# Kernel optimization log

Measured on AMD Instinct MI355X. Metric: run time of the kernel, lower is better.

Reference implementation:

```python
import jax, jax.numpy as jnp
import numpy as np


COMMITMENT_COST = 0.25


def setup_inputs() -> dict:
    key = jax.random.key(0)
    k1, k2 = jax.random.split(key)
    B, C, H, W = 16, 128, 64, 64
    K = 1024
    z = jax.random.normal(k1, (B, C, H, W), dtype=jnp.float32)
    # original init: uniform(-1/K, 1/K); keep that scale for faithfulness
    codebook = jax.random.uniform(k2, (K, C), dtype=jnp.float32,
                                  minval=-1.0 / K, maxval=1.0 / K)
    return {"z": z, "codebook": codebook}


def reference(z, codebook):
    B, C, H, W = z.shape
    K = codebook.shape[0]
    # (B,C,H,W) -> (N,C) with N = B*H*W
    z_flat = jnp.transpose(z, (0, 2, 3, 1)).reshape(-1, C)
    # squared-distance matrix (N,K): ||z||^2 + ||e||^2 - 2 z.e
    dists = (jnp.sum(z_flat ** 2, axis=1, keepdims=True)
             + jnp.sum(codebook ** 2, axis=1)
             - 2.0 * z_flat @ codebook.T)
    indices = jnp.argmin(dists, axis=1)  # (N,)
    z_q = jnp.transpose(codebook[indices].reshape(B, H, W, C), (0, 3, 1, 2))
    commitment_loss = jnp.mean((jax.lax.stop_gradient(z_q) - z) ** 2)
    codebook_loss = jnp.mean((z_q - jax.lax.stop_gradient(z)) ** 2)
    vq_loss = codebook_loss + COMMITMENT_COST * commitment_loss
    # straight-through estimator
    z_q_st = z + jax.lax.stop_gradient(z_q - z)
    usage = jnp.sum(jnp.bincount(indices, length=K) > 0).astype(jnp.float32) / K
    return (z_q_st, vq_loss, usage)
```

## Files before the change

kernel.cpp:

```cpp
#include <hip/hip_runtime.h>

typedef __attribute__((ext_vector_type(8))) short short8;
typedef __attribute__((ext_vector_type(4))) float f32x4;

#define C_DIM 128
#define K_CODES 1024
#define TOT 8388608
#define NBLK 512

__device__ __forceinline__ unsigned int f2bf1(float f) {
  unsigned int u = __float_as_uint(f);
  return (u + 0x7FFFu + ((u >> 16) & 1u)) >> 16;
}
__device__ __forceinline__ unsigned int f2bf2(float lo, float hi) {
  return f2bf1(lo) | (f2bf1(hi) << 16);
}

union U16x8 { uint4 u; short8 s; };

__global__ void prep_kernel(const float* __restrict__ cb,
                            unsigned short* __restrict__ ebf,
                            float* __restrict__ nsq1,
                            int* __restrict__ used) {
  int gid = blockIdx.x * 256 + threadIdx.x;
  const float4 v = ((const float4*)cb)[gid];
  uint2 pk;
  pk.x = f2bf2(v.x, v.y);
  pk.y = f2bf2(v.z, v.w);
  ((uint2*)ebf)[gid] = pk;
  if (gid < K_CODES) {
    float s = 0.f;
    #pragma unroll 8
    for (int c = 0; c < C_DIM; ++c) { float w = cb[gid * C_DIM + c]; s += w * w; }
    nsq1[gid] = 1.0f + s;
    used[gid] = 0;
  }
}

__global__ __launch_bounds__(512, 4)
void vq_main(const float* __restrict__ zin,
             const unsigned short* __restrict__ ebf,
             const float* __restrict__ nsq1,
             int* __restrict__ used, float* __restrict__ lossp,
             float* __restrict__ out) {
  __shared__ __align__(16) uint4 bG[2][1024];
  __shared__ float nsq_s[K_CODES];
  __shared__ unsigned int mergeK[128][2];
  __shared__ int   widx[128];
  __shared__ float wsum[8];

  const int t  = threadIdx.x;
  const int L  = t & 63;
  const int wv = t >> 6;
  const int ph = wv >> 1;
  const int kh = wv & 1;
  const int q  = L >> 4;
  const int nL = L & 15;

  const int bb = blockIdx.x >> 5;
  const int hg = blockIdx.x & 31;
  const int zoff = bb * (C_DIM * 4096) + hg * 128;

  for (int i = t; i < K_CODES; i += 512) nsq_s[i] = nsq1[i];

  short8 afrag[8];
  #pragma unroll
  for (int mt = 0; mt < 2; ++mt) {
    const int wcol = ph * 32 + mt * 16 + nL;
    #pragma unroll
    for (int ks = 0; ks < 4; ++ks) {
      float v[8];
      #pragma unroll
      for (int u = 0; u < 8; ++u)
        v[u] = zin[zoff + (ks * 32 + q * 8 + u) * 4096 + wcol];
      U16x8 pk;
      pk.u.x = f2bf2(-2.f * v[0], -2.f * v[1]);
      pk.u.y = f2bf2(-2.f * v[2], -2.f * v[3]);
      pk.u.z = f2bf2(-2.f * v[4], -2.f * v[5]);
      pk.u.w = f2bf2(-2.f * v[6], -2.f * v[7]);
      afrag[mt * 4 + ks] = pk.s;
    }
  }

  const uint4* __restrict__ ebv = (const uint4*)ebf;
  const int nLw = (t >> 4) & 15;
  const int oct = t & 15;
  const int pb  = t >> 8;
  const int sks = oct >> 2, sq = oct & 3;

  #pragma unroll
  for (int i = 0; i < 2; ++i) {
    int p = pb + 2 * i;
    bG[0][p * 256 + sks * 64 + nLw * 4 + sq] = ebv[(p * 16 + nLw) * 16 + oct];
  }
  __syncthreads();

  unsigned int kmin[8];
  #pragma unroll
  for (int i = 0; i < 8; ++i) kmin[i] = 0xFFFFFFFFu;

  #pragma unroll 1
  for (int ch = 0; ch < 16; ++ch) {
    const int cur = ch & 1;
    if (ch < 15) {
      #pragma unroll
      for (int i = 0; i < 2; ++i) {
        int p = pb + 2 * i;
        bG[cur ^ 1][p * 256 + sks * 64 + nLw * 4 + sq] =
            ebv[((ch + 1) * 64 + p * 16 + nLw) * 16 + oct];
      }
    }
    const short8* bp = (const short8*)bG[cur];
    #pragma unroll
    for (int j2 = 0; j2 < 2; ++j2) {
      const int jj = kh * 2 + j2;
      const int row = ch * 64 + jj * 16 + nL;
      short8 b0 = bp[jj * 256 + 0 * 64 + nL * 4 + q];
      short8 b1 = bp[jj * 256 + 1 * 64 + nL * 4 + q];
      short8 b2 = bp[jj * 256 + 2 * 64 + nL * 4 + q];
      short8 b3 = bp[jj * 256 + 3 * 64 + nL * 4 + q];
      const float nv = nsq_s[row];
      f32x4 c0 = {nv, nv, nv, nv};
      f32x4 c1 = {nv, nv, nv, nv};
      c0 = __builtin_amdgcn_mfma_f32_16x16x32_bf16(afrag[0], b0, c0, 0, 0, 0);
      c1 = __builtin_amdgcn_mfma_f32_16x16x32_bf16(afrag[4], b0, c1, 0, 0, 0);
      c0 = __builtin_amdgcn_mfma_f32_16x16x32_bf16(afrag[1], b1, c0, 0, 0, 0);
      c1 = __builtin_amdgcn_mfma_f32_16x16x32_bf16(afrag[5], b1, c1, 0, 0, 0);
      c0 = __builtin_amdgcn_mfma_f32_16x16x32_bf16(afrag[2], b2, c0, 0, 0, 0);
      c1 = __builtin_amdgcn_mfma_f32_16x16x32_bf16(afrag[6], b2, c1, 0, 0, 0);
      c0 = __builtin_amdgcn_mfma_f32_16x16x32_bf16(afrag[3], b3, c0, 0, 0, 0);
      c1 = __builtin_amdgcn_mfma_f32_16x16x32_bf16(afrag[7], b3, c1, 0, 0, 0);
      const unsigned int rowc = (unsigned int)row;
      #pragma unroll
      for (int r = 0; r < 4; ++r) {
        unsigned int k0 = (__float_as_uint(c0[r]) & 0xFFFFFC00u) | rowc;
        if (k0 < kmin[r]) kmin[r] = k0;
        unsigned int k1 = (__float_as_uint(c1[r]) & 0xFFFFFC00u) | rowc;
        if (k1 < kmin[4 + r]) kmin[4 + r] = k1;
      }
    }
    __syncthreads();
  }

  #pragma unroll
  for (int m = 1; m <= 8; m <<= 1) {
    #pragma unroll
    for (int i = 0; i < 8; ++i) {
      unsigned int o = (unsigned int)__shfl_xor((int)kmin[i], m, 64);
      if (o < kmin[i]) kmin[i] = o;
    }
  }
  if (nL == 0) {
    #pragma unroll
    for (int mt = 0; mt < 2; ++mt)
      #pragma unroll
      for (int r = 0; r < 4; ++r)
        mergeK[ph * 32 + mt * 16 + q * 4 + r][kh] = kmin[mt * 4 + r];
  }
  __syncthreads();

  if (t < 128) {
    unsigned int b = min(mergeK[t][0], mergeK[t][1]);
    int bi = (int)(b & 1023u);
    widx[t] = bi;
    used[bi] = 1;
  }
  __syncthreads();

  float lsum = 0.f;
  {
    const int p = t & 127, cg = t >> 7;
    const int idx = widx[p];
    const uint4* erow = ebv + idx * 16 + cg * 4;
    const int obase = zoff + cg * 32 * 4096 + p;
    #pragma unroll
    for (int i = 0; i < 4; ++i) {
      uint4 g = erow[i];
      const unsigned int wrd[4] = {g.x, g.y, g.z, g.w};
      #pragma unroll
      for (int half = 0; half < 4; ++half) {
        float e0 = __uint_as_float(wrd[half] << 16);
        float e1 = __uint_as_float(wrd[half] & 0xFFFF0000u);
        int off = obase + (i * 8 + half * 2) * 4096;
        float d0 = zin[off] - e0;
        out[off] = e0;
        lsum += d0 * d0;
        off += 4096;
        float d1 = zin[off] - e1;
        out[off] = e1;
        lsum += d1 * d1;
      }
    }
  }
  #pragma unroll
  for (int o = 32; o > 0; o >>= 1) lsum += __shfl_down(lsum, o, 64);
  if (L == 0) wsum[wv] = lsum;
  __syncthreads();
  if (t == 0)
    lossp[blockIdx.x] = ((wsum[0] + wsum[1]) + (wsum[2] + wsum[3]))
                      + ((wsum[4] + wsum[5]) + (wsum[6] + wsum[7]));
}

__global__ void finalize_kernel(const int* __restrict__ used,
                                const float* __restrict__ lossp,
                                float* __restrict__ out2) {
  __shared__ int   redi[256];
  __shared__ float redf[256];
  int t = threadIdx.x;
  int s = 0;
  for (int i = t; i < K_CODES; i += 256) s += (used[i] != 0) ? 1 : 0;
  float ls = 0.f;
  for (int i = t; i < NBLK; i += 256) ls += lossp[i];
  redi[t] = s; redf[t] = ls;
  __syncthreads();
  for (int o = 128; o > 0; o >>= 1) {
    if (t < o) { redi[t] += redi[t + o]; redf[t] += redf[t + o]; }
    __syncthreads();
  }
  if (t == 0) {
    out2[0] = 1.25f * redf[0] / (float)TOT;
    out2[1] = (float)redi[0] / 1024.0f;
  }
}

extern "C" void kernel_launch(void* const* d_in, const int* in_sizes, int n_in,
                              void* d_out, int out_size, void* d_ws, size_t ws_size,
                              hipStream_t stream) {
  const float* z  = (const float*)d_in[0];
  const float* cb = (const float*)d_in[1];
  float* out = (float*)d_out;
  char* ws = (char*)d_ws;
  unsigned short* ebf = (unsigned short*)ws;
  float* nsq1  = (float*)(ws + 262144);
  int*   used  = (int*)(ws + 266240);
  float* lossp = (float*)(ws + 270336);

  hipLaunchKernelGGL(prep_kernel, dim3(128), dim3(256), 0, stream,
                     cb, ebf, nsq1, used);
  hipLaunchKernelGGL(vq_main, dim3(NBLK), dim3(512), 0, stream,
                     z, ebf, nsq1, used, lossp, out);
  hipLaunchKernelGGL(finalize_kernel, dim3(1), dim3(256), 0, stream,
                     used, lossp, out + TOT);
}
```

Measured before the change: 116.9 us.

## Widen per-wave M tile to 64 rows and swizzle LDS codebook layout

Each wave now holds A fragments for 64 pixel columns (four M tiles) and covers one 16-code slice per chunk, instead of 32 columns and two code slices. Every B fragment read from LDS now feeds four MFMAs rather than two, which halves LDS read traffic per MFMA. The shared codebook tile is also stored with an XOR swizzle to cut bank conflicts, and the final argmin merge combines four partial results instead of two. In exchange, register pressure roughly doubles for A fragments, accumulators and kmin values, which could cause spills or reduce occupancy under the 512x4 launch bounds.

New measurement: 117.8 us. About the same (+0.8%).

```diff
diff --git a/kernel.cpp b/kernel.cpp
--- a/kernel.cpp
+++ b/kernel.cpp
@@ -45,15 +45,15 @@
              float* __restrict__ out) {
   __shared__ __align__(16) uint4 bG[2][1024];
   __shared__ float nsq_s[K_CODES];
-  __shared__ unsigned int mergeK[128][2];
+  __shared__ unsigned int mergeK[128][4];
   __shared__ int   widx[128];
   __shared__ float wsum[8];
 
   const int t  = threadIdx.x;
   const int L  = t & 63;
   const int wv = t >> 6;
-  const int ph = wv >> 1;
-  const int kh = wv & 1;
+  const int ph = wv >> 2;
+  const int kq = wv & 3;
   const int q  = L >> 4;
   const int nL = L & 15;
 
@@ -63,10 +63,10 @@
 
   for (int i = t; i < K_CODES; i += 512) nsq_s[i] = nsq1[i];
 
-  short8 afrag[8];
-  #pragma unroll
-  for (int mt = 0; mt < 2; ++mt) {
-    const int wcol = ph * 32 + mt * 16 + nL;
+  short8 afrag[16];
+  #pragma unroll
+  for (int mt = 0; mt < 4; ++mt) {
+    const int wcol = ph * 64 + mt * 16 + nL;
     #pragma unroll
     for (int ks = 0; ks < 4; ++ks) {
       float v[8];
@@ -87,17 +87,23 @@
   const int oct = t & 15;
   const int pb  = t >> 8;
   const int sks = oct >> 2, sq = oct & 3;
+  const int swbase = (nLw >> 1) * 8 + (((nLw ^ sks) & 1) << 2)
+                   + ((sq ^ (nLw >> 1)) & 3);
 
   #pragma unroll
   for (int i = 0; i < 2; ++i) {
     int p = pb + 2 * i;
-    bG[0][p * 256 + sks * 64 + nLw * 4 + sq] = ebv[(p * 16 + nLw) * 16 + oct];
-  }
-  __syncthreads();
-
-  unsigned int kmin[8];
-  #pragma unroll
-  for (int i = 0; i < 8; ++i) kmin[i] = 0xFFFFFFFFu;
+    bG[0][p * 256 + sks * 64 + swbase] = ebv[(p * 16 + nLw) * 16 + oct];
+  }
+  __syncthreads();
+
+  const int rdq = (q ^ (nL >> 1)) & 3;
+  const int sA = kq * 256 + (nL >> 1) * 8 + (((nL) & 1) << 2) + rdq;
+  const int sB = kq * 256 + (nL >> 1) * 8 + (((nL ^ 1) & 1) << 2) + rdq;
+
+  unsigned int kmin[16];
+  #pragma unroll
+  for (int i = 0; i < 16; ++i) kmin[i] = 0xFFFFFFFFu;
 
   #pragma unroll 1
   for (int ch = 0; ch < 16; ++ch) {
@@ -106,30 +112,38 @@
       #pragma unroll
       for (int i = 0; i < 2; ++i) {
         int p = pb + 2 * i;
-        bG[cur ^ 1][p * 256 + sks * 64 + nLw * 4 + sq] =
+        bG[cur ^ 1][p * 256 + sks * 64 + swbase] =
             ebv[((ch + 1) * 64 + p * 16 + nLw) * 16 + oct];
       }
     }
     const short8* bp = (const short8*)bG[cur];
-    #pragma unroll
-    for (int j2 = 0; j2 < 2; ++j2) {
-      const int jj = kh * 2 + j2;
-      const int row = ch * 64 + jj * 16 + nL;
-      short8 b0 = bp[jj * 256 + 0 * 64 + nL * 4 + q];
-      short8 b1 = bp[jj * 256 + 1 * 64 + nL * 4 + q];
-      short8 b2 = bp[jj * 256 + 2 * 64 + nL * 4 + q];
-      short8 b3 = bp[jj * 256 + 3 * 64 + nL * 4 + q];
+    {
+      const int row = ch * 64 + kq * 16 + nL;
+      short8 b0 = bp[sA];
+      short8 b1 = bp[sB + 64];
+      short8 b2 = bp[sA + 128];
+      short8 b3 = bp[sB + 192];
       const float nv = nsq_s[row];
       f32x4 c0 = {nv, nv, nv, nv};
       f32x4 c1 = {nv, nv, nv, nv};
-      c0 = __builtin_amdgcn_mfma_f32_16x16x32_bf16(afrag[0], b0, c0, 0, 0, 0);
-      c1 = __builtin_amdgcn_mfma_f32_16x16x32_bf16(afrag[4], b0, c1, 0, 0, 0);
-      c0 = __builtin_amdgcn_mfma_f32_16x16x32_bf16(afrag[1], b1, c0, 0, 0, 0);
-      c1 = __builtin_amdgcn_mfma_f32_16x16x32_bf16(afrag[5], b1, c1, 0, 0, 0);
-      c0 = __builtin_amdgcn_mfma_f32_16x16x32_bf16(afrag[2], b2, c0, 0, 0, 0);
-      c1 = __builtin_amdgcn_mfma_f32_16x16x32_bf16(afrag[6], b2, c1, 0, 0, 0);
-      c0 = __builtin_amdgcn_mfma_f32_16x16x32_bf16(afrag[3], b3, c0, 0, 0, 0);
-      c1 = __builtin_amdgcn_mfma_f32_16x16x32_bf16(afrag[7], b3, c1, 0, 0, 0);
+      f32x4 c2 = {nv, nv, nv, nv};
+      f32x4 c3 = {nv, nv, nv, nv};
+      c0 = __builtin_amdgcn_mfma_f32_16x16x32_bf16(afrag[0],  b0, c0, 0, 0, 0);
+      c1 = __builtin_amdgcn_mfma_f32_16x16x32_bf16(afrag[4],  b0, c1, 0, 0, 0);
+      c2 = __builtin_amdgcn_mfma_f32_16x16x32_bf16(afrag[8],  b0, c2, 0, 0, 0);
+      c3 = __builtin_amdgcn_mfma_f32_16x16x32_bf16(afrag[12], b0, c3, 0, 0, 0);
+      c0 = __builtin_amdgcn_mfma_f32_16x16x32_bf16(afrag[1],  b1, c0, 0, 0, 0);
+      c1 = __builtin_amdgcn_mfma_f32_16x16x32_bf16(afrag[5],  b1, c1, 0, 0, 0);
+      c2 = __builtin_amdgcn_mfma_f32_16x16x32_bf16(afrag[9],  b1, c2, 0, 0, 0);
+      c3 = __builtin_amdgcn_mfma_f32_16x16x32_bf16(afrag[13], b1, c3, 0, 0, 0);
+      c0 = __builtin_amdgcn_mfma_f32_16x16x32_bf16(afrag[2],  b2, c0, 0, 0, 0);
+      c1 = __builtin_amdgcn_mfma_f32_16x16x32_bf16(afrag[6],  b2, c1, 0, 0, 0);
+      c2 = __builtin_amdgcn_mfma_f32_16x16x32_bf16(afrag[10], b2, c2, 0, 0, 0);
+      c3 = __builtin_amdgcn_mfma_f32_16x16x32_bf16(afrag[14], b2, c3, 0, 0, 0);
+      c0 = __builtin_amdgcn_mfma_f32_16x16x32_bf16(afrag[3],  b3, c0, 0, 0, 0);
+      c1 = __builtin_amdgcn_mfma_f32_16x16x32_bf16(afrag[7],  b3, c1, 0, 0, 0);
+      c2 = __builtin_amdgcn_mfma_f32_16x16x32_bf16(afrag[11], b3, c2, 0, 0, 0);
+      c3 = __builtin_amdgcn_mfma_f32_16x16x32_bf16(afrag[15], b3, c3, 0, 0, 0);
       const unsigned int rowc = (unsigned int)row;
       #pragma unroll
       for (int r = 0; r < 4; ++r) {
@@ -137,6 +151,10 @@
         if (k0 < kmin[r]) kmin[r] = k0;
         unsigned int k1 = (__float_as_uint(c1[r]) & 0xFFFFFC00u) | rowc;
         if (k1 < kmin[4 + r]) kmin[4 + r] = k1;
+        unsigned int k2 = (__float_as_uint(c2[r]) & 0xFFFFFC00u) | rowc;
+        if (k2 < kmin[8 + r]) kmin[8 + r] = k2;
+        unsigned int k3 = (__float_as_uint(c3[r]) & 0xFFFFFC00u) | rowc;
+        if (k3 < kmin[12 + r]) kmin[12 + r] = k3;
       }
     }
     __syncthreads();
@@ -145,22 +163,23 @@
   #pragma unroll
   for (int m = 1; m <= 8; m <<= 1) {
     #pragma unroll
-    for (int i = 0; i < 8; ++i) {
+    for (int i = 0; i < 16; ++i) {
       unsigned int o = (unsigned int)__shfl_xor((int)kmin[i], m, 64);
       if (o < kmin[i]) kmin[i] = o;
     }
   }
   if (nL == 0) {
     #pragma unroll
-    for (int mt = 0; mt < 2; ++mt)
+    for (int mt = 0; mt < 4; ++mt)
       #pragma unroll
       for (int r = 0; r < 4; ++r)
-        mergeK[ph * 32 + mt * 16 + q * 4 + r][kh] = kmin[mt * 4 + r];
+        mergeK[ph * 64 + mt * 16 + q * 4 + r][kq] = kmin[mt * 4 + r];
   }
   __syncthreads();
 
   if (t < 128) {
-    unsigned int b = min(mergeK[t][0], mergeK[t][1]);
+    unsigned int b = min(min(mergeK[t][0], mergeK[t][1]),
+                         min(mergeK[t][2], mergeK[t][3]));
     int bi = (int)(b & 1023u);
     widx[t] = bi;
     used[bi] = 1;
@@ -171,7 +190,7 @@
   {
     const int p = t & 127, cg = t >> 7;
     const int idx = widx[p];
-    const uint4* erow = ebv + idx * 16 + cg * 4;
+    const uint4* erow = (const uint4*)ebf + idx * 16 + cg * 4;
     const int obase = zoff + cg * 32 * 4096 + p;
     #pragma unroll
     for (int i = 0; i < 4; ++i) {
```
